# Kernel tuning notes

Hardware: AMD Instinct MI355X
Metric: run time of the kernel (lower is better)

The kernel has to match this reference:

```python
import jax, jax.numpy as jnp
import numpy as np

N = 100000      # n_nodes
E = 3200000     # n_edges (avg degree 32)
F_IN = 256
H = 64
H2 = 32
C = 2
EPS = 1e-5      # BatchNorm eps


def setup_inputs() -> dict:
    key = jax.random.key(0)
    ks = jax.random.split(key, 16)
    x = jax.random.normal(ks[0], (N, F_IN), jnp.float32)
    edge_index = jax.random.randint(ks[1], (2, E), 0, N, jnp.int32)
    # GCNConv params (glorot-ish scaling)
    W1 = jax.random.normal(ks[2], (F_IN, H), jnp.float32) / np.sqrt(F_IN)
    b1 = jnp.zeros((H,), jnp.float32)
    W2 = jax.random.normal(ks[3], (H, H2), jnp.float32) / np.sqrt(H)
    b2 = jnp.zeros((H2,), jnp.float32)
    Wl = jax.random.normal(ks[4], (H2, C), jnp.float32) / np.sqrt(H2)
    bl = jnp.zeros((C,), jnp.float32)
    # BatchNorm affine + running stats (eval mode)
    gamma1 = 1.0 + 0.1 * jax.random.normal(ks[5], (H,), jnp.float32)
    beta1 = 0.1 * jax.random.normal(ks[6], (H,), jnp.float32)
    mean1 = 0.1 * jax.random.normal(ks[7], (H,), jnp.float32)
    var1 = jax.random.uniform(ks[8], (H,), jnp.float32, 0.5, 1.5)
    gamma2 = 1.0 + 0.1 * jax.random.normal(ks[9], (H2,), jnp.float32)
    beta2 = 0.1 * jax.random.normal(ks[10], (H2,), jnp.float32)
    mean2 = 0.1 * jax.random.normal(ks[11], (H2,), jnp.float32)
    var2 = jax.random.uniform(ks[12], (H2,), jnp.float32, 0.5, 1.5)
    return dict(x=x, edge_index=edge_index, W1=W1, b1=b1, gamma1=gamma1,
                beta1=beta1, mean1=mean1, var1=var1, W2=W2, b2=b2,
                gamma2=gamma2, beta2=beta2, mean2=mean2, var2=var2,
                Wl=Wl, bl=bl)


def _gcn_conv(x, src, dst, W, b):
    # PyG GCNConv: transform first, then normalized aggregation w/ self-loops
    h = x @ W                                              # [N, out]
    deg = jax.ops.segment_sum(jnp.ones((E,), h.dtype), dst, num_segments=N) + 1.0
    dinv = jax.lax.rsqrt(deg)                              # deg^-1/2 incl self-loop
    norm = dinv[src] * dinv[dst]                           # [E]
    agg = jax.ops.segment_sum(h[src] * norm[:, None], dst, num_segments=N)
    agg = agg + h * (dinv * dinv)[:, None]                 # self-loop messages
    return agg + b


def _bn(x, gamma, beta, mean, var):
    return (x - mean) * jax.lax.rsqrt(var + EPS) * gamma + beta


def reference(x, edge_index, W1, b1, gamma1, beta1, mean1, var1,
              W2, b2, gamma2, beta2, mean2, var2, Wl, bl):
    src, dst = edge_index[0], edge_index[1]
    h = _gcn_conv(x, src, dst, W1, b1)
    h = jax.nn.relu(_bn(h, gamma1, beta1, mean1, var1))    # dropout: eval -> identity
    h = _gcn_conv(h, src, dst, W2, b2)
    h = jax.nn.relu(_bn(h, gamma2, beta2, mean2, var2))
    return h @ Wl + bl
```

## Files before the change

kernel.cpp:

```cpp
#include <hip/hip_runtime.h>
#include <hip/hip_fp16.h>

#define N_NODES 100000
#define N_EDGES 3200000
#define F_IN 256
#define H1 64
#define H2C 32
#define NCLS 2
#define EPS 1e-5f

#define NBK 391
#define BK_CAP 10240
#define SCHUNK 16384

#define KPAD 264
#define WPAD 40

typedef _Float16 f16x8 __attribute__((ext_vector_type(8)));
typedef float f32x4 __attribute__((ext_vector_type(4)));

__global__ __launch_bounds__(256) void k_bin_count(const int* __restrict__ dst,
                                                   int* __restrict__ bucket_count) {
    __shared__ int h[NBK];
    for (int i = threadIdx.x; i < NBK; i += 256) h[i] = 0;
    __syncthreads();
    int stride = gridDim.x * 256;
    for (int e = blockIdx.x * 256 + threadIdx.x; e < N_EDGES; e += stride)
        atomicAdd(&h[((unsigned)dst[e]) >> 8], 1);
    __syncthreads();
    for (int i = threadIdx.x; i < NBK; i += 256)
        if (h[i]) atomicAdd(&bucket_count[i], h[i]);
}

__global__ void k_bucket_scan(const int* __restrict__ bucket_count,
                              int* __restrict__ bucket_base) {
    __shared__ int s[512];
    int t = threadIdx.x;
    int v = (t < NBK) ? bucket_count[t] : 0;
    s[t] = v;
    __syncthreads();
    for (int off = 1; off < 512; off <<= 1) {
        int x = (t >= off) ? s[t - off] : 0;
        __syncthreads();
        s[t] += x;
        __syncthreads();
    }
    if (t < NBK) bucket_base[t] = s[t] - v;
    if (t == 0) bucket_base[NBK] = N_EDGES;
}

__global__ __launch_bounds__(256) void k_bin_scatter(const int* __restrict__ src,
                                                     const int* __restrict__ dst,
                                                     const int* __restrict__ bucket_base,
                                                     int* __restrict__ cursor,
                                                     int* __restrict__ packed) {
    __shared__ int h[NBK];
    __shared__ int base[NBK];
    int t = threadIdx.x;
    int e0 = blockIdx.x * SCHUNK;
    int e1 = e0 + SCHUNK; if (e1 > N_EDGES) e1 = N_EDGES;
    for (int i = t; i < NBK; i += 256) h[i] = 0;
    __syncthreads();
    for (int e = e0 + t; e < e1; e += 256)
        atomicAdd(&h[((unsigned)dst[e]) >> 8], 1);
    __syncthreads();
    for (int i = t; i < NBK; i += 256) {
        int c = h[i];
        base[i] = c ? (bucket_base[i] + atomicAdd(&cursor[i], c)) : 0;
        h[i] = 0;
    }
    __syncthreads();
    for (int e = e0 + t; e < e1; e += 256) {
        int d = dst[e];
        int b = ((unsigned)d) >> 8;
        int pos = base[b] + atomicAdd(&h[b], 1);
        packed[pos] = ((d & 255) << 24) | src[e];
    }
}

__global__ __launch_bounds__(256) void k_csr_build(const int* __restrict__ packed,
                                                   const int* __restrict__ bucket_base,
                                                   int* __restrict__ csr,
                                                   int* __restrict__ offs_g,
                                                   float* __restrict__ dinv) {
    __shared__ int hist[256];
    __shared__ int offs[257];
    __shared__ int csr_l[BK_CAP];
    int t = threadIdx.x;
    int b = blockIdx.x;
    int node0 = b << 8;
    int nn = N_NODES - node0; if (nn > 256) nn = 256;
    int ebase = bucket_base[b];
    int ecnt = bucket_base[b + 1] - ebase;
    if (ecnt > BK_CAP) ecnt = BK_CAP;

    hist[t] = 0;
    __syncthreads();
    for (int i = t; i < ecnt; i += 256)
        atomicAdd(&hist[((unsigned)packed[ebase + i]) >> 24], 1);
    __syncthreads();
    int d = hist[t];
    offs[t] = d;
    __syncthreads();
    for (int off = 1; off < 256; off <<= 1) {
        int x = (t >= off) ? offs[t - off] : 0;
        __syncthreads();
        offs[t] += x;
        __syncthreads();
    }
    int incl = offs[t];
    int excl = incl - d;
    __syncthreads();
    offs[t] = excl;
    if (t == 255) offs[256] = incl;
    hist[t] = 0;
    __syncthreads();
    for (int i = t; i < ecnt; i += 256) {
        int p = packed[ebase + i];
        int ld = ((unsigned)p) >> 24;
        int pos = offs[ld] + atomicAdd(&hist[ld], 1);
        csr_l[pos] = p & 0xFFFFFF;
    }
    __syncthreads();
    for (int i = t; i < ecnt; i += 256)
        csr[ebase + i] = csr_l[i];
    if (t < nn) {
        offs_g[node0 + t] = ebase + excl;
        dinv[node0 + t] = rsqrtf((float)d + 1.0f);
    }
    if (b == NBK - 1 && t == 0) offs_g[N_NODES] = N_EDGES;
}

__global__ __launch_bounds__(256) void k_gemm1m(const float* __restrict__ x,
                                                const float* __restrict__ W1,
                                                const float* __restrict__ dinv,
                                                unsigned short* __restrict__ h1s) {
    __shared__ __align__(16) unsigned short xt[64 * KPAD];
    __shared__ __align__(16) unsigned short wtc[64 * WPAD];
    int t = threadIdx.x;
    int lane = t & 63;
    int w = t >> 6;
    int nodeBase = blockIdx.x * 64;

    #pragma unroll
    for (int i = 0; i < 16; i++) {
        int f = i * 256 + t;
        int node = f >> 6;
        int pos = f & 63;
        int gn = nodeBase + node; if (gn >= N_NODES) gn = N_NODES - 1;
        float4 v = *(const float4*)(x + (size_t)gn * F_IN + pos * 4);
        ushort4 h;
        h.x = __half_as_ushort(__float2half(v.x));
        h.y = __half_as_ushort(__float2half(v.y));
        h.z = __half_as_ushort(__float2half(v.z));
        h.w = __half_as_ushort(__float2half(v.w));
        *(ushort4*)&xt[node * KPAD + pos * 4] = h;
    }
    f32x4 acc0 = {}, acc1 = {}, acc2 = {}, acc3 = {};
    __syncthreads();

    int am = lane & 15;
    int ag = lane >> 4;
    for (int kc = 0; kc < 8; kc++) {
        #pragma unroll
        for (int i = 0; i < 2; i++) {
            int f = i * 256 + t;
            int kk = f >> 4;
            int c4 = (f & 15) * 4;
            float4 v = *(const float4*)(W1 + (size_t)(kc * 32 + kk) * H1 + c4);
            wtc[(c4 + 0) * WPAD + kk] = __half_as_ushort(__float2half(v.x));
            wtc[(c4 + 1) * WPAD + kk] = __half_as_ushort(__float2half(v.y));
            wtc[(c4 + 2) * WPAD + kk] = __half_as_ushort(__float2half(v.z));
            wtc[(c4 + 3) * WPAD + kk] = __half_as_ushort(__float2half(v.w));
        }
        __syncthreads();
        f16x8 a = *(const f16x8*)&xt[(w * 16 + am) * KPAD + kc * 32 + ag * 8];
        f16x8 b0 = *(const f16x8*)&wtc[(0 * 16 + am) * WPAD + ag * 8];
        f16x8 b1 = *(const f16x8*)&wtc[(1 * 16 + am) * WPAD + ag * 8];
        f16x8 b2 = *(const f16x8*)&wtc[(2 * 16 + am) * WPAD + ag * 8];
        f16x8 b3 = *(const f16x8*)&wtc[(3 * 16 + am) * WPAD + ag * 8];
        acc0 = __builtin_amdgcn_mfma_f32_16x16x32_f16(a, b0, acc0, 0, 0, 0);
        acc1 = __builtin_amdgcn_mfma_f32_16x16x32_f16(a, b1, acc1, 0, 0, 0);
        acc2 = __builtin_amdgcn_mfma_f32_16x16x32_f16(a, b2, acc2, 0, 0, 0);
        acc3 = __builtin_amdgcn_mfma_f32_16x16x32_f16(a, b3, acc3, 0, 0, 0);
        __syncthreads();
    }

    #pragma unroll
    for (int r = 0; r < 4; r++) {
        int node = nodeBase + w * 16 + ag * 4 + r;
        if (node < N_NODES) {
            float dn = dinv[node];
            unsigned short* orow = &h1s[(size_t)node * H1];
            orow[ 0 + am] = __half_as_ushort(__float2half(acc0[r] * dn));
            orow[16 + am] = __half_as_ushort(__float2half(acc1[r] * dn));
            orow[32 + am] = __half_as_ushort(__float2half(acc2[r] * dn));
            orow[48 + am] = __half_as_ushort(__float2half(acc3[r] * dn));
        }
    }
}

__global__ __launch_bounds__(256) void k_agg1f(const unsigned short* __restrict__ h1s,
                                               const float* __restrict__ dinv,
                                               const int* __restrict__ offs,
                                               const int* __restrict__ csr,
                                               const float* __restrict__ b1,
                                               const float* __restrict__ g1,
                                               const float* __restrict__ be1,
                                               const float* __restrict__ m1,
                                               const float* __restrict__ v1,
                                               const float* __restrict__ W2,
                                               unsigned short* __restrict__ h2s) {
    __shared__ float w2[H1 * H2C];
    __shared__ float rows[8][64];
    int t = threadIdx.x;
    for (int i = t; i < H1 * H2C; i += 256) w2[i] = W2[i];
    __syncthreads();

    int slot = t >> 5;
    int cp = t & 31;
    int n = blockIdx.x * 8 + slot;
    const ushort2* hp = (const ushort2*)h1s;
    float sx = 0.f, sy = 0.f;
    int k = offs[n], kend = offs[n + 1];
    for (; k + 15 < kend; k += 16) {
        int s0 = csr[k],      s1 = csr[k + 1],  s2 = csr[k + 2],  s3 = csr[k + 3];
        int s4 = csr[k + 4],  s5 = csr[k + 5],  s6 = csr[k + 6],  s7 = csr[k + 7];
        int s8 = csr[k + 8],  s9 = csr[k + 9],  sa = csr[k + 10], sb = csr[k + 11];
        int sc = csr[k + 12], sd = csr[k + 13], se = csr[k + 14], sf = csr[k + 15];
        ushort2 u0 = hp[(size_t)s0 * 32 + cp], u1 = hp[(size_t)s1 * 32 + cp];
        ushort2 u2 = hp[(size_t)s2 * 32 + cp], u3 = hp[(size_t)s3 * 32 + cp];
        ushort2 u4 = hp[(size_t)s4 * 32 + cp], u5 = hp[(size_t)s5 * 32 + cp];
        ushort2 u6 = hp[(size_t)s6 * 32 + cp], u7 = hp[(size_t)s7 * 32 + cp];
        ushort2 u8 = hp[(size_t)s8 * 32 + cp], u9 = hp[(size_t)s9 * 32 + cp];
        ushort2 ua = hp[(size_t)sa * 32 + cp], ub = hp[(size_t)sb * 32 + cp];
        ushort2 uc = hp[(size_t)sc * 32 + cp], ud = hp[(size_t)sd * 32 + cp];
        ushort2 ue = hp[(size_t)se * 32 + cp], uf = hp[(size_t)sf * 32 + cp];
        float2 f0 = __half22float2(*(const __half2*)&u0);
        float2 f1 = __half22float2(*(const __half2*)&u1);
        float2 f2 = __half22float2(*(const __half2*)&u2);
        float2 f3 = __half22float2(*(const __half2*)&u3);
        float2 f4 = __half22float2(*(const __half2*)&u4);
        float2 f5 = __half22float2(*(const __half2*)&u5);
        float2 f6 = __half22float2(*(const __half2*)&u6);
        float2 f7 = __half22float2(*(const __half2*)&u7);
        float2 f8 = __half22float2(*(const __half2*)&u8);
        float2 f9 = __half22float2(*(const __half2*)&u9);
        float2 fa = __half22float2(*(const __half2*)&ua);
        float2 fb = __half22float2(*(const __half2*)&ub);
        float2 fc = __half22float2(*(const __half2*)&uc);
        float2 fd = __half22float2(*(const __half2*)&ud);
        float2 fe = __half22float2(*(const __half2*)&ue);
        float2 ff = __half22float2(*(const __half2*)&uf);
        sx += ((f0.x + f1.x) + (f2.x + f3.x)) + ((f4.x + f5.x) + (f6.x + f7.x))
            + ((f8.x + f9.x) + (fa.x + fb.x)) + ((fc.x + fd.x) + (fe.x + ff.x));
        sy += ((f0.y + f1.y) + (f2.y + f3.y)) + ((f4.y + f5.y) + (f6.y + f7.y))
            + ((f8.y + f9.y) + (fa.y + fb.y)) + ((fc.y + fd.y) + (fe.y + ff.y));
    }
    for (; k + 7 < kend; k += 8) {
        int s0 = csr[k],     s1 = csr[k + 1], s2 = csr[k + 2], s3 = csr[k + 3];
        int s4 = csr[k + 4], s5 = csr[k + 5], s6 = csr[k + 6], s7 = csr[k + 7];
        ushort2 u0 = hp[(size_t)s0 * 32 + cp], u1 = hp[(size_t)s1 * 32 + cp];
        ushort2 u2 = hp[(size_t)s2 * 32 + cp], u3 = hp[(size_t)s3 * 32 + cp];
        ushort2 u4 = hp[(size_t)s4 * 32 + cp], u5 = hp[(size_t)s5 * 32 + cp];
        ushort2 u6 = hp[(size_t)s6 * 32 + cp], u7 = hp[(size_t)s7 * 32 + cp];
        float2 f0 = __half22float2(*(const __half2*)&u0);
        float2 f1 = __half22float2(*(const __half2*)&u1);
        float2 f2 = __half22float2(*(const __half2*)&u2);
        float2 f3 = __half22float2(*(const __half2*)&u3);
        float2 f4 = __half22float2(*(const __half2*)&u4);
        float2 f5 = __half22float2(*(const __half2*)&u5);
        float2 f6 = __half22float2(*(const __half2*)&u6);
        float2 f7 = __half22float2(*(const __half2*)&u7);
        sx += (f0.x + f1.x) + (f2.x + f3.x) + ((f4.x + f5.x) + (f6.x + f7.x));
        sy += (f0.y + f1.y) + (f2.y + f3.y) + ((f4.y + f5.y) + (f6.y + f7.y));
    }
    if (k < kend) {
        int last = kend - 1;
        int i1 = k + 1 <= last ? k + 1 : last;
        int i2 = k + 2 <= last ? k + 2 : last;
        int i3 = k + 3 <= last ? k + 3 : last;
        int i4 = k + 4 <= last ? k + 4 : last;
        int i5 = k + 5 <= last ? k + 5 : last;
        int i6 = k + 6 <= last ? k + 6 : last;
        int s0 = csr[k],  s1 = csr[i1], s2 = csr[i2], s3 = csr[i3];
        int s4 = csr[i4], s5 = csr[i5], s6 = csr[i6];
        ushort2 u0 = hp[(size_t)s0 * 32 + cp], u1 = hp[(size_t)s1 * 32 + cp];
        ushort2 u2 = hp[(size_t)s2 * 32 + cp], u3 = hp[(size_t)s3 * 32 + cp];
        ushort2 u4 = hp[(size_t)s4 * 32 + cp], u5 = hp[(size_t)s5 * 32 + cp];
        ushort2 u6 = hp[(size_t)s6 * 32 + cp];
        float2 f0 = __half22float2(*(const __half2*)&u0);
        float2 f1 = __half22float2(*(const __half2*)&u1);
        float2 f2 = __half22float2(*(const __half2*)&u2);
        float2 f3 = __half22float2(*(const __half2*)&u3);
        float2 f4 = __half22float2(*(const __half2*)&u4);
        float2 f5 = __half22float2(*(const __half2*)&u5);
        float2 f6 = __half22float2(*(const __half2*)&u6);
        float m1v = (k + 1 <= last) ? 1.f : 0.f;
        float m2v = (k + 2 <= last) ? 1.f : 0.f;
        float m3v = (k + 3 <= last) ? 1.f : 0.f;
        float m4v = (k + 4 <= last) ? 1.f : 0.f;
        float m5v = (k + 5 <= last) ? 1.f : 0.f;
        float m6v = (k + 6 <= last) ? 1.f : 0.f;
        sx += f0.x + m1v * f1.x + m2v * f2.x + m3v * f3.x + m4v * f4.x + m5v * f5.x + m6v * f6.x;
        sy += f0.y + m1v * f1.y + m2v * f2.y + m3v * f3.y + m4v * f4.y + m5v * f5.y + m6v * f6.y;
    }
    ushort2 su = hp[(size_t)n * 32 + cp];
    float2 sf2 = __half22float2(*(const __half2*)&su);
    float dn = dinv[n];
    int c0 = cp * 2, c1 = c0 + 1;
    float r0 = (sx + sf2.x) * dn + b1[c0];
    float r1 = (sy + sf2.y) * dn + b1[c1];
    r0 = (r0 - m1[c0]) * rsqrtf(v1[c0] + EPS) * g1[c0] + be1[c0];
    r1 = (r1 - m1[c1]) * rsqrtf(v1[c1] + EPS) * g1[c1] + be1[c1];
    rows[slot][c0] = fmaxf(r0, 0.f);
    rows[slot][c1] = fmaxf(r1, 0.f);
    __syncthreads();
    const float4* rp = (const float4*)rows[slot];
    float acc = 0.f;
    #pragma unroll
    for (int q = 0; q < 16; q++) {
        float4 rv = rp[q];
        int kb = q * 4;
        acc += rv.x * w2[(kb + 0) * H2C + cp] + rv.y * w2[(kb + 1) * H2C + cp]
             + rv.z * w2[(kb + 2) * H2C + cp] + rv.w * w2[(kb + 3) * H2C + cp];
    }
    h2s[(size_t)n * H2C + cp] = __half_as_ushort(__float2half(acc * dn));
}

__global__ __launch_bounds__(256) void k_agg2(const unsigned short* __restrict__ h2s,
                                              const float* __restrict__ dinv,
                                              const int* __restrict__ offs,
                                              const int* __restrict__ csr,
                                              const float* __restrict__ b2,
                                              const float* __restrict__ g2,
                                              const float* __restrict__ be2,
                                              const float* __restrict__ m2,
                                              const float* __restrict__ v2,
                                              const float* __restrict__ Wl,
                                              const float* __restrict__ bl,
                                              float* __restrict__ out) {
    int gid = blockIdx.x * 256 + threadIdx.x;
    int n = gid >> 4;
    int cp = gid & 15;
    if (n >= N_NODES) return;
    const ushort2* hp = (const ushort2*)h2s;
    float sx = 0.f, sy = 0.f;
    int k = offs[n], kend = offs[n + 1];
    for (; k + 15 < kend; k += 16) {
        int s0 = csr[k],      s1 = csr[k + 1],  s2 = csr[k + 2],  s3 = csr[k + 3];
        int s4 = csr[k + 4],  s5 = csr[k + 5],  s6 = csr[k + 6],  s7 = csr[k + 7];
        int s8 = csr[k + 8],  s9 = csr[k + 9],  sa = csr[k + 10], sb = csr[k + 11];
        int sc = csr[k + 12], sd = csr[k + 13], se = csr[k + 14], sf = csr[k + 15];
        ushort2 u0 = hp[(size_t)s0 * 16 + cp], u1 = hp[(size_t)s1 * 16 + cp];
        ushort2 u2 = hp[(size_t)s2 * 16 + cp], u3 = hp[(size_t)s3 * 16 + cp];
        ushort2 u4 = hp[(size_t)s4 * 16 + cp], u5 = hp[(size_t)s5 * 16 + cp];
        ushort2 u6 = hp[(size_t)s6 * 16 + cp], u7 = hp[(size_t)s7 * 16 + cp];
        ushort2 u8 = hp[(size_t)s8 * 16 + cp], u9 = hp[(size_t)s9 * 16 + cp];
        ushort2 ua = hp[(size_t)sa * 16 + cp], ub = hp[(size_t)sb * 16 + cp];
        ushort2 uc = hp[(size_t)sc * 16 + cp], ud = hp[(size_t)sd * 16 + cp];
        ushort2 ue = hp[(size_t)se * 16 + cp], uf = hp[(size_t)sf * 16 + cp];
        float2 f0 = __half22float2(*(const __half2*)&u0);
        float2 f1 = __half22float2(*(const __half2*)&u1);
        float2 f2 = __half22float2(*(const __half2*)&u2);
        float2 f3 = __half22float2(*(const __half2*)&u3);
        float2 f4 = __half22float2(*(const __half2*)&u4);
        float2 f5 = __half22float2(*(const __half2*)&u5);
        float2 f6 = __half22float2(*(const __half2*)&u6);
        float2 f7 = __half22float2(*(const __half2*)&u7);
        float2 f8 = __half22float2(*(const __half2*)&u8);
        float2 f9 = __half22float2(*(const __half2*)&u9);
        float2 fa = __half22float2(*(const __half2*)&ua);
        float2 fb = __half22float2(*(const __half2*)&ub);
        float2 fc = __half22float2(*(const __half2*)&uc);
        float2 fd = __half22float2(*(const __half2*)&ud);
        float2 fe = __half22float2(*(const __half2*)&ue);
        float2 ff = __half22float2(*(const __half2*)&uf);
        sx += ((f0.x + f1.x) + (f2.x + f3.x)) + ((f4.x + f5.x) + (f6.x + f7.x))
            + ((f8.x + f9.x) + (fa.x + fb.x)) + ((fc.x + fd.x) + (fe.x + ff.x));
        sy += ((f0.y + f1.y) + (f2.y + f3.y)) + ((f4.y + f5.y) + (f6.y + f7.y))
            + ((f8.y + f9.y) + (fa.y + fb.y)) + ((fc.y + fd.y) + (fe.y + ff.y));
    }
    for (; k + 7 < kend; k += 8) {
        int s0 = csr[k],     s1 = csr[k + 1], s2 = csr[k + 2], s3 = csr[k + 3];
        int s4 = csr[k + 4], s5 = csr[k + 5], s6 = csr[k + 6], s7 = csr[k + 7];
        ushort2 u0 = hp[(size_t)s0 * 16 + cp], u1 = hp[(size_t)s1 * 16 + cp];
        ushort2 u2 = hp[(size_t)s2 * 16 + cp], u3 = hp[(size_t)s3 * 16 + cp];
        ushort2 u4 = hp[(size_t)s4 * 16 + cp], u5 = hp[(size_t)s5 * 16 + cp];
        ushort2 u6 = hp[(size_t)s6 * 16 + cp], u7 = hp[(size_t)s7 * 16 + cp];
        float2 f0 = __half22float2(*(const __half2*)&u0);
        float2 f1 = __half22float2(*(const __half2*)&u1);
        float2 f2 = __half22float2(*(const __half2*)&u2);
        float2 f3 = __half22float2(*(const __half2*)&u3);
        float2 f4 = __half22float2(*(const __half2*)&u4);
        float2 f5 = __half22float2(*(const __half2*)&u5);
        float2 f6 = __half22float2(*(const __half2*)&u6);
        float2 f7 = __half22float2(*(const __half2*)&u7);
        sx += (f0.x + f1.x) + (f2.x + f3.x) + ((f4.x + f5.x) + (f6.x + f7.x));
        sy += (f0.y + f1.y) + (f2.y + f3.y) + ((f4.y + f5.y) + (f6.y + f7.y));
    }
    if (k < kend) {
        int last = kend - 1;
        int i1 = k + 1 <= last ? k + 1 : last;
        int i2 = k + 2 <= last ? k + 2 : last;
        int i3 = k + 3 <= last ? k + 3 : last;
        int i4 = k + 4 <= last ? k + 4 : last;
        int i5 = k + 5 <= last ? k + 5 : last;
        int i6 = k + 6 <= last ? k + 6 : last;
        int s0 = csr[k],  s1 = csr[i1], s2 = csr[i2], s3 = csr[i3];
        int s4 = csr[i4], s5 = csr[i5], s6 = csr[i6];
        ushort2 u0 = hp[(size_t)s0 * 16 + cp], u1 = hp[(size_t)s1 * 16 + cp];
        ushort2 u2 = hp[(size_t)s2 * 16 + cp], u3 = hp[(size_t)s3 * 16 + cp];
        ushort2 u4 = hp[(size_t)s4 * 16 + cp], u5 = hp[(size_t)s5 * 16 + cp];
        ushort2 u6 = hp[(size_t)s6 * 16 + cp];
        float2 f0 = __half22float2(*(const __half2*)&u0);
        float2 f1 = __half22float2(*(const __half2*)&u1);
        float2 f2 = __half22float2(*(const __half2*)&u2);
        float2 f3 = __half22float2(*(const __half2*)&u3);
        float2 f4 = __half22float2(*(const __half2*)&u4);
        float2 f5 = __half22float2(*(const __half2*)&u5);
        float2 f6 = __half22float2(*(const __half2*)&u6);
        float m1v = (k + 1 <= last) ? 1.f : 0.f;
        float m2v = (k + 2 <= last) ? 1.f : 0.f;
        float m3v = (k + 3 <= last) ? 1.f : 0.f;
        float m4v = (k + 4 <= last) ? 1.f : 0.f;
        float m5v = (k + 5 <= last) ? 1.f : 0.f;
        float m6v = (k + 6 <= last) ? 1.f : 0.f;
        sx += f0.x + m1v * f1.x + m2v * f2.x + m3v * f3.x + m4v * f4.x + m5v * f5.x + m6v * f6.x;
        sy += f0.y + m1v * f1.y + m2v * f2.y + m3v * f3.y + m4v * f4.y + m5v * f5.y + m6v * f6.y;
    }
    ushort2 su = hp[(size_t)n * 16 + cp];
    float2 sf2 = __half22float2(*(const __half2*)&su);
    float dn = dinv[n];
    int c0 = cp * 2, c1 = c0 + 1;
    float r0 = (sx + sf2.x) * dn + b2[c0];
    float r1 = (sy + sf2.y) * dn + b2[c1];
    r0 = (r0 - m2[c0]) * rsqrtf(v2[c0] + EPS) * g2[c0] + be2[c0];
    r1 = (r1 - m2[c1]) * rsqrtf(v2[c1] + EPS) * g2[c1] + be2[c1];
    r0 = fmaxf(r0, 0.f);
    r1 = fmaxf(r1, 0.f);
    float p0 = r0 * Wl[c0 * 2 + 0] + r1 * Wl[c1 * 2 + 0];
    float p1 = r0 * Wl[c0 * 2 + 1] + r1 * Wl[c1 * 2 + 1];
    #pragma unroll
    for (int off = 8; off > 0; off >>= 1) {
        p0 += __shfl_xor(p0, off);
        p1 += __shfl_xor(p1, off);
    }
    if (cp == 0) {
        *(float2*)&out[(size_t)n * NCLS] = make_float2(p0 + bl[0], p1 + bl[1]);
    }
}

extern "C" void kernel_launch(void* const* d_in, const int* in_sizes, int n_in,
                              void* d_out, int out_size, void* d_ws, size_t ws_size,
                              hipStream_t stream) {
    const float* x   = (const float*)d_in[0];
    const int*   ei  = (const int*)d_in[1];
    const int*   src = ei;
    const int*   dst = ei + N_EDGES;
    const float* W1  = (const float*)d_in[2];
    const float* b1  = (const float*)d_in[3];
    const float* g1  = (const float*)d_in[4];
    const float* be1 = (const float*)d_in[5];
    const float* m1  = (const float*)d_in[6];
    const float* v1  = (const float*)d_in[7];
    const float* W2  = (const float*)d_in[8];
    const float* b2  = (const float*)d_in[9];
    const float* g2  = (const float*)d_in[10];
    const float* be2 = (const float*)d_in[11];
    const float* m2  = (const float*)d_in[12];
    const float* v2  = (const float*)d_in[13];
    const float* Wl  = (const float*)d_in[14];
    const float* bl  = (const float*)d_in[15];
    float* out = (float*)d_out;

    char* p = (char*)d_ws;
    int*   bucket_count = (int*)p;  p += 1600;
    int*   cursor       = (int*)p;  p += 1600;
    int*   bucket_base  = (int*)p;  p += 1600;
    int*   offs         = (int*)p;  p += 400016;
    float* dinv         = (float*)p; p += 400000;
    int*   packed       = (int*)p;  p += (size_t)N_EDGES * 4;
    int*   csr          = (int*)p;  p += (size_t)N_EDGES * 4;
    unsigned short* h1s = (unsigned short*)p; p += (size_t)N_NODES * H1 * 2;
    unsigned short* h2s = (unsigned short*)p; p += (size_t)N_NODES * H2C * 2;

    hipMemsetAsync(bucket_count, 0, 3200, stream);

    k_bin_count<<<512, 256, 0, stream>>>(dst, bucket_count);
    k_bucket_scan<<<1, 512, 0, stream>>>(bucket_count, bucket_base);
    k_bin_scatter<<<(N_EDGES + SCHUNK - 1) / SCHUNK, 256, 0, stream>>>(src, dst, bucket_base, cursor, packed);
    k_csr_build<<<NBK, 256, 0, stream>>>(packed, bucket_base, csr, offs, dinv);
    k_gemm1m<<<(N_NODES + 63) / 64, 256, 0, stream>>>(x, W1, dinv, h1s);
    k_agg1f<<<N_NODES / 8, 256, 0, stream>>>(h1s, dinv, offs, csr, b1, g1, be1, m1, v1, W2, h2s);
    k_agg2<<<(N_NODES * 16) / 256, 256, 0, stream>>>(h2s, dinv, offs, csr, b2, g2, be2, m2, v2, Wl, bl, out);
}
```

Before: 266.7 us.

## Partially sort CSR neighbors by source range and relax row barrier to wave barrier

The CSR build now buckets each destination's neighbor list into four coarse source-index ranges (src>>15) using a 1024-entry histogram. The scan runs over per-node totals, and each node's sub-bucket offsets are derived from it. The aim is to make the later gathers of h[src] in the aggregation kernels more cache-local. Separately, a block-wide __syncthreads in the agg1 epilogue is replaced by a wave barrier, which is only correct if each row slot is written and read within a single wavefront.

Result: no change. 265.8 us (-0.3%).

```diff
diff --git a/kernel.cpp b/kernel.cpp
--- a/kernel.cpp
+++ b/kernel.cpp
@@ -83,8 +83,8 @@
                                                    int* __restrict__ csr,
                                                    int* __restrict__ offs_g,
                                                    float* __restrict__ dinv) {
-    __shared__ int hist[256];
-    __shared__ int offs[257];
+    __shared__ int hist[1024];
+    __shared__ int nsum[256];
     __shared__ int csr_l[BK_CAP];
     int t = threadIdx.x;
     int b = blockIdx.x;
@@ -94,32 +94,38 @@
     int ecnt = bucket_base[b + 1] - ebase;
     if (ecnt > BK_CAP) ecnt = BK_CAP;
 
-    hist[t] = 0;
-    __syncthreads();
-    for (int i = t; i < ecnt; i += 256)
-        atomicAdd(&hist[((unsigned)packed[ebase + i]) >> 24], 1);
-    __syncthreads();
-    int d = hist[t];
-    offs[t] = d;
-    __syncthreads();
-    for (int off = 1; off < 256; off <<= 1) {
-        int x = (t >= off) ? offs[t - off] : 0;
-        __syncthreads();
-        offs[t] += x;
-        __syncthreads();
-    }
-    int incl = offs[t];
-    int excl = incl - d;
-    __syncthreads();
-    offs[t] = excl;
-    if (t == 255) offs[256] = incl;
-    hist[t] = 0;
+    for (int i = t; i < 1024; i += 256) hist[i] = 0;
     __syncthreads();
     for (int i = t; i < ecnt; i += 256) {
         int p = packed[ebase + i];
         int ld = ((unsigned)p) >> 24;
-        int pos = offs[ld] + atomicAdd(&hist[ld], 1);
-        csr_l[pos] = p & 0xFFFFFF;
+        int sl = (p & 0xFFFFFF) >> 15;
+        atomicAdd(&hist[ld * 4 + sl], 1);
+    }
+    __syncthreads();
+    int c0 = hist[t * 4 + 0], c1 = hist[t * 4 + 1];
+    int c2 = hist[t * 4 + 2], c3 = hist[t * 4 + 3];
+    int d = c0 + c1 + c2 + c3;
+    nsum[t] = d;
+    __syncthreads();
+    for (int off = 1; off < 256; off <<= 1) {
+        int x = (t >= off) ? nsum[t - off] : 0;
+        __syncthreads();
+        nsum[t] += x;
+        __syncthreads();
+    }
+    int excl = nsum[t] - d;
+    hist[t * 4 + 0] = excl;
+    hist[t * 4 + 1] = excl + c0;
+    hist[t * 4 + 2] = excl + c0 + c1;
+    hist[t * 4 + 3] = excl + c0 + c1 + c2;
+    __syncthreads();
+    for (int i = t; i < ecnt; i += 256) {
+        int p = packed[ebase + i];
+        int ld = ((unsigned)p) >> 24;
+        int srcv = p & 0xFFFFFF;
+        int pos = atomicAdd(&hist[ld * 4 + (srcv >> 15)], 1);
+        csr_l[pos] = srcv;
     }
     __syncthreads();
     for (int i = t; i < ecnt; i += 256)
@@ -315,7 +321,7 @@
     r1 = (r1 - m1[c1]) * rsqrtf(v1[c1] + EPS) * g1[c1] + be1[c1];
     rows[slot][c0] = fmaxf(r0, 0.f);
     rows[slot][c1] = fmaxf(r1, 0.f);
-    __syncthreads();
+    __builtin_amdgcn_wave_barrier();
     const float4* rp = (const float4*)rows[slot];
     float acc = 0.f;
     #pragma unroll
```

## Replace counted bucket scan with fixed-capacity buckets and per-node end offsets

Applied to the files above, without the earlier changes.

Drops the bin-count and bucket-scan kernels by giving each destination bucket a fixed-capacity slot (BK_CAP) and using the atomic cursor count directly as the bucket size. Adds a per-node end-offset array so the aggregation kernels no longer rely on contiguous CSR offsets. Also doubles the scatter chunk size, makes the x loads in the GEMM nontemporal, and swaps a block barrier for a wave barrier in agg1f. This saves one full pass over dst and two launches, but edges are silently truncated if any bucket exceeds BK_CAP, and the wave barrier is only safe if each slot's row is written and read by a single wavefront.

After: 291.3 us. 1.09x slower.

```diff
diff --git a/kernel.cpp b/kernel.cpp
--- a/kernel.cpp
+++ b/kernel.cpp
@@ -11,49 +11,19 @@
 
 #define NBK 391
 #define BK_CAP 10240
-#define SCHUNK 16384
+#define SCHUNK 32768
 
 #define KPAD 264
 #define WPAD 40
 
 typedef _Float16 f16x8 __attribute__((ext_vector_type(8)));
 typedef float f32x4 __attribute__((ext_vector_type(4)));
-
-__global__ __launch_bounds__(256) void k_bin_count(const int* __restrict__ dst,
-                                                   int* __restrict__ bucket_count) {
-    __shared__ int h[NBK];
-    for (int i = threadIdx.x; i < NBK; i += 256) h[i] = 0;
-    __syncthreads();
-    int stride = gridDim.x * 256;
-    for (int e = blockIdx.x * 256 + threadIdx.x; e < N_EDGES; e += stride)
-        atomicAdd(&h[((unsigned)dst[e]) >> 8], 1);
-    __syncthreads();
-    for (int i = threadIdx.x; i < NBK; i += 256)
-        if (h[i]) atomicAdd(&bucket_count[i], h[i]);
-}
-
-__global__ void k_bucket_scan(const int* __restrict__ bucket_count,
-                              int* __restrict__ bucket_base) {
-    __shared__ int s[512];
-    int t = threadIdx.x;
-    int v = (t < NBK) ? bucket_count[t] : 0;
-    s[t] = v;
-    __syncthreads();
-    for (int off = 1; off < 512; off <<= 1) {
-        int x = (t >= off) ? s[t - off] : 0;
-        __syncthreads();
-        s[t] += x;
-        __syncthreads();
-    }
-    if (t < NBK) bucket_base[t] = s[t] - v;
-    if (t == 0) bucket_base[NBK] = N_EDGES;
-}
-
-__global__ __launch_bounds__(256) void k_bin_scatter(const int* __restrict__ src,
-                                                     const int* __restrict__ dst,
-                                                     const int* __restrict__ bucket_base,
-                                                     int* __restrict__ cursor,
-                                                     int* __restrict__ packed) {
+typedef float fvec4 __attribute__((ext_vector_type(4)));
+
+__global__ __launch_bounds__(256) void k_scatter1p(const int* __restrict__ src,
+                                                   const int* __restrict__ dst,
+                                                   int* __restrict__ cursor,
+                                                   int* __restrict__ packed) {
     __shared__ int h[NBK];
     __shared__ int base[NBK];
     int t = threadIdx.x;
@@ -66,7 +36,7 @@
     __syncthreads();
     for (int i = t; i < NBK; i += 256) {
         int c = h[i];
-        base[i] = c ? (bucket_base[i] + atomicAdd(&cursor[i], c)) : 0;
+        base[i] = c ? (i * BK_CAP + atomicAdd(&cursor[i], c)) : 0;
         h[i] = 0;
     }
     __syncthreads();
@@ -79,9 +49,10 @@
 }
 
 __global__ __launch_bounds__(256) void k_csr_build(const int* __restrict__ packed,
-                                                   const int* __restrict__ bucket_base,
+                                                   const int* __restrict__ cursor,
                                                    int* __restrict__ csr,
                                                    int* __restrict__ offs_g,
+                                                   int* __restrict__ endx_g,
                                                    float* __restrict__ dinv) {
     __shared__ int hist[256];
     __shared__ int offs[257];
@@ -90,8 +61,8 @@
     int b = blockIdx.x;
     int node0 = b << 8;
     int nn = N_NODES - node0; if (nn > 256) nn = 256;
-    int ebase = bucket_base[b];
-    int ecnt = bucket_base[b + 1] - ebase;
+    int ebase = b * BK_CAP;
+    int ecnt = cursor[b];
     if (ecnt > BK_CAP) ecnt = BK_CAP;
 
     hist[t] = 0;
@@ -126,9 +97,9 @@
         csr[ebase + i] = csr_l[i];
     if (t < nn) {
         offs_g[node0 + t] = ebase + excl;
+        endx_g[node0 + t] = ebase + incl;
         dinv[node0 + t] = rsqrtf((float)d + 1.0f);
     }
-    if (b == NBK - 1 && t == 0) offs_g[N_NODES] = N_EDGES;
 }
 
 __global__ __launch_bounds__(256) void k_gemm1m(const float* __restrict__ x,
@@ -148,7 +119,7 @@
         int node = f >> 6;
         int pos = f & 63;
         int gn = nodeBase + node; if (gn >= N_NODES) gn = N_NODES - 1;
-        float4 v = *(const float4*)(x + (size_t)gn * F_IN + pos * 4);
+        fvec4 v = __builtin_nontemporal_load((const fvec4*)(x + (size_t)gn * F_IN + pos * 4));
         ushort4 h;
         h.x = __half_as_ushort(__float2half(v.x));
         h.y = __half_as_ushort(__float2half(v.y));
@@ -203,6 +174,7 @@
 __global__ __launch_bounds__(256) void k_agg1f(const unsigned short* __restrict__ h1s,
                                                const float* __restrict__ dinv,
                                                const int* __restrict__ offs,
+                                               const int* __restrict__ endx,
                                                const int* __restrict__ csr,
                                                const float* __restrict__ b1,
                                                const float* __restrict__ g1,
@@ -222,7 +194,7 @@
     int n = blockIdx.x * 8 + slot;
     const ushort2* hp = (const ushort2*)h1s;
     float sx = 0.f, sy = 0.f;
-    int k = offs[n], kend = offs[n + 1];
+    int k = offs[n], kend = endx[n];
     for (; k + 15 < kend; k += 16) {
         int s0 = csr[k],      s1 = csr[k + 1],  s2 = csr[k + 2],  s3 = csr[k + 3];
         int s4 = csr[k + 4],  s5 = csr[k + 5],  s6 = csr[k + 6],  s7 = csr[k + 7];
@@ -315,7 +287,7 @@
     r1 = (r1 - m1[c1]) * rsqrtf(v1[c1] + EPS) * g1[c1] + be1[c1];
     rows[slot][c0] = fmaxf(r0, 0.f);
     rows[slot][c1] = fmaxf(r1, 0.f);
-    __syncthreads();
+    __builtin_amdgcn_wave_barrier();
     const float4* rp = (const float4*)rows[slot];
     float acc = 0.f;
     #pragma unroll
@@ -331,6 +303,7 @@
 __global__ __launch_bounds__(256) void k_agg2(const unsigned short* __restrict__ h2s,
                                               const float* __restrict__ dinv,
                                               const int* __restrict__ offs,
+                                              const int* __restrict__ endx,
                                               const int* __restrict__ csr,
                                               const float* __restrict__ b2,
                                               const float* __restrict__ g2,
@@ -346,7 +319,7 @@
     if (n >= N_NODES) return;
     const ushort2* hp = (const ushort2*)h2s;
     float sx = 0.f, sy = 0.f;
-    int k = offs[n], kend = offs[n + 1];
+    int k = offs[n], kend = endx[n];
     for (; k + 15 < kend; k += 16) {
         int s0 = csr[k],      s1 = csr[k + 1],  s2 = csr[k + 2],  s3 = csr[k + 3];
         int s4 = csr[k + 4],  s5 = csr[k + 5],  s6 = csr[k + 6],  s7 = csr[k + 7];
@@ -475,23 +448,20 @@
     float* out = (float*)d_out;
 
     char* p = (char*)d_ws;
-    int*   bucket_count = (int*)p;  p += 1600;
-    int*   cursor       = (int*)p;  p += 1600;
-    int*   bucket_base  = (int*)p;  p += 1600;
-    int*   offs         = (int*)p;  p += 400016;
-    float* dinv         = (float*)p; p += 400000;
-    int*   packed       = (int*)p;  p += (size_t)N_EDGES * 4;
-    int*   csr          = (int*)p;  p += (size_t)N_EDGES * 4;
+    int*   cursor  = (int*)p;  p += 1600;
+    int*   offs    = (int*)p;  p += 400000;
+    int*   endx    = (int*)p;  p += 400000;
+    float* dinv    = (float*)p; p += 400000;
+    int*   packed  = (int*)p;  p += (size_t)NBK * BK_CAP * 4;
+    int*   csr     = (int*)p;  p += (size_t)NBK * BK_CAP * 4;
     unsigned short* h1s = (unsigned short*)p; p += (size_t)N_NODES * H1 * 2;
     unsigned short* h2s = (unsigned short*)p; p += (size_t)N_NODES * H2C * 2;
 
-    hipMemsetAsync(bucket_count, 0, 3200, stream);
-
-    k_bin_count<<<512, 256, 0, stream>>>(dst, bucket_count);
-    k_bucket_scan<<<1, 512, 0, stream>>>(bucket_count, bucket_base);
-    k_bin_scatter<<<(N_EDGES + SCHUNK - 1) / SCHUNK, 256, 0, stream>>>(src, dst, bucket_base, cursor, packed);
-    k_csr_build<<<NBK, 256, 0, stream>>>(packed, bucket_base, csr, offs, dinv);
+    (void)hipMemsetAsync(cursor, 0, 1600, stream);
+
+    k_scatter1p<<<(N_EDGES + SCHUNK - 1) / SCHUNK, 256, 0, stream>>>(src, dst, cursor, packed);
+    k_csr_build<<<NBK, 256, 0, stream>>>(packed, cursor, csr, offs, endx, dinv);
     k_gemm1m<<<(N_NODES + 63) / 64, 256, 0, stream>>>(x, W1, dinv, h1s);
-    k_agg1f<<<N_NODES / 8, 256, 0, stream>>>(h1s, dinv, offs, csr, b1, g1, be1, m1, v1, W2, h2s);
-    k_agg2<<<(N_NODES * 16) / 256, 256, 0, stream>>>(h2s, dinv, offs, csr, b2, g2, be2, m2, v2, Wl, bl, out);
-}
+    k_agg1f<<<N_NODES / 8, 256, 0, stream>>>(h1s, dinv, offs, endx, csr, b1, g1, be1, m1, v1, W2, h2s);
+    k_agg2<<<(N_NODES * 16) / 256, 256, 0, stream>>>(h2s, dinv, offs, endx, csr, b2, g2, be2, m2, v2, Wl, bl, out);
+}
```
